# Kernel optimization log

Hardware: AMD Instinct MI355X
Metric: run time of the kernel (lower is better)

The kernel has to match this reference:

```python
import jax, jax.numpy as jnp
import numpy as np

ATTWSIZE = 64  # sliding window length (matches init_kwargs attwsize)


def setup_inputs() -> dict:
    key = jax.random.key(0)
    k1, k2, k3 = jax.random.split(key, 3)
    B, T, D, A = 32, 4096, 256, 128
    x = jax.random.normal(k1, (B, T, D), dtype=jnp.float32)
    Wp = jax.random.normal(k2, (A, D), dtype=jnp.float32) / np.sqrt(D).astype(np.float32)
    bp = jnp.zeros((A,), dtype=jnp.float32)
    Wg = jax.random.normal(k3, (1, A), dtype=jnp.float32) / np.sqrt(A).astype(np.float32)
    return {"x": x, "Wp": Wp, "bp": bp, "Wg": Wg}


def _windowed_sum(v, w):
    # causal sliding-window sum over axis=1: sum(v[:, max(t-w+1,0):t+1, :])
    # single-pass cumsum formulation: cs[t] - cs[t-w]
    cs = jnp.cumsum(v, axis=1)
    T = v.shape[1]
    shifted = jnp.pad(cs, ((0, 0), (w, 0), (0, 0)))[:, :T, :]
    return cs - shifted


def reference(x, Wp, bp, Wg):
    # proj = tanh(Linear(dimio->dimatt)(x))
    proj = jnp.tanh(jnp.einsum('btd,ad->bta', x, Wp) + bp)
    # gvec = sigmoid(Linear(dimatt->1, no bias)(proj))  -> [B, T, 1]
    g = jax.nn.sigmoid(jnp.einsum('bta,oa->bto', proj, Wg))
    wx = g * x  # gated input [B, T, D]
    num = _windowed_sum(wx, ATTWSIZE)         # [B, T, D]
    den = _windowed_sum(g, ATTWSIZE)          # [B, T, 1] broadcasts over D
    return num / den
```

## Files before the change

kernel.cpp:

```cpp
#include <hip/hip_runtime.h>

#define TT 4096
#define DD 256
#define AA 128
#define WIN 64

typedef short bf16x8 __attribute__((ext_vector_type(8)));
typedef float f32x4 __attribute__((ext_vector_type(4)));
typedef unsigned int u32x4 __attribute__((ext_vector_type(4)));

__device__ __forceinline__ unsigned short f2bf(float f) {
    unsigned int u = __builtin_bit_cast(unsigned int, f);
    u += 0x7FFFu + ((u >> 16) & 1u);
    return (unsigned short)(u >> 16);
}

__device__ __forceinline__ unsigned int cvt_pk_bf16(float lo, float hi) {
    unsigned int r;
    asm("v_cvt_pk_bf16_f32 %0, %1, %2" : "=v"(r) : "v"(lo), "v"(hi));
    return r;
}

__global__ __launch_bounds__(256) void prep_wp(const float* __restrict__ Wp,
                                               unsigned short* __restrict__ wpb) {
    int i = blockIdx.x * 256 + threadIdx.x;
    wpb[i] = f2bf(Wp[i]);
}

#define SROWS 32
#define TC    256
#define NU    ((TC + WIN) / SROWS)
#define NCHK  (TT / TC)

__global__ __launch_bounds__(256, 2) void fused_kernel(
        const float* __restrict__ x, const unsigned short* __restrict__ wpb,
        const float* __restrict__ bp, const float* __restrict__ Wg,
        float* __restrict__ out) {
    __shared__ __align__(16) float xs[2][SROWS * DD];
    __shared__ float gbuf[4][SROWS];
    __shared__ float psum[4][SROWS];
    const int tid  = threadIdx.x;
    const int lane = tid & 63;
    const int wave = tid >> 6;
    const int quad = lane >> 4;
    const int nrow = lane & 15;
    const int sw   = nrow & 7;
    const int b     = blockIdx.x >> 4;
    const int chunk = blockIdx.x & (NCHK - 1);
    const long t0   = (long)chunk * TC;
    const float* xb = x   + (size_t)b * TT * DD;
    float*       ob = out + (size_t)b * TT * DD;

    bf16x8 bfrag[2][8];
    float bpv[2], wgv[2];
#pragma unroll
    for (int nt = 0; nt < 2; ++nt) {
        int n = wave * 32 + nt * 16 + nrow;
        bpv[nt] = bp[n];
        wgv[nt] = Wg[n];
#pragma unroll
        for (int k0 = 0; k0 < 8; ++k0)
            bfrag[nt][k0] = *reinterpret_cast<const bf16x8*>(
                wpb + n * DD + k0 * 32 + quad * 8);
    }

    auto stage = [&](int su) {
        const int nb = su & 1;
        const long r0 = t0 - WIN + (long)su * SROWS;
#pragma unroll
        for (int j = 0; j < 8; ++j) {
            int r = wave * 8 + j;
            long row = r0 + r;
            row = row < 0 ? 0 : row;
            const float* gp = xb + row * DD + ((lane ^ (r & 7)) << 2);
            __builtin_amdgcn_global_load_lds(
                (const __attribute__((address_space(1))) void*)gp,
                (__attribute__((address_space(3))) void*)&xs[nb][r * DD],
                16, 0, 0);
        }
    };

    float S = 0.f, Sg = 0.f;

    stage(0);

    for (int u = 0; u <= NU; ++u) {
        if (u + 1 < NU) stage(u + 1);

        if (u + 1 < NU) asm volatile("s_waitcnt vmcnt(8) lgkmcnt(0)" ::: "memory");
        else            asm volatile("s_waitcnt vmcnt(0) lgkmcnt(0)" ::: "memory");
        __builtin_amdgcn_sched_barrier(0);
        __builtin_amdgcn_s_barrier();
        __builtin_amdgcn_sched_barrier(0);

        if (u < NU) {
            const float* buf = xs[u & 1];
            f32x4 acc[2][2];
#pragma unroll
            for (int mt = 0; mt < 2; ++mt)
#pragma unroll
                for (int nt = 0; nt < 2; ++nt)
                    acc[mt][nt] = (f32x4){0.f, 0.f, 0.f, 0.f};
#pragma unroll
            for (int k0 = 0; k0 < 8; ++k0) {
#pragma unroll
                for (int mt = 0; mt < 2; ++mt) {
                    const float* rowp = buf + (mt * 16 + nrow) * DD;
                    const int gidx = quad * 2 + k0 * 8;
                    float4 f0 = *reinterpret_cast<const float4*>(rowp + (((gidx)     ^ sw) << 2));
                    float4 f1 = *reinterpret_cast<const float4*>(rowp + (((gidx + 1) ^ sw) << 2));
                    u32x4 w;
                    w.x = cvt_pk_bf16(f0.x, f0.y);
                    w.y = cvt_pk_bf16(f0.z, f0.w);
                    w.z = cvt_pk_bf16(f1.x, f1.y);
                    w.w = cvt_pk_bf16(f1.z, f1.w);
                    bf16x8 af = __builtin_bit_cast(bf16x8, w);
                    acc[mt][0] = __builtin_amdgcn_mfma_f32_16x16x32_bf16(af, bfrag[0][k0], acc[mt][0], 0, 0, 0);
                    acc[mt][1] = __builtin_amdgcn_mfma_f32_16x16x32_bf16(af, bfrag[1][k0], acc[mt][1], 0, 0, 0);
                }
            }
            float p[2][4];
#pragma unroll
            for (int mt = 0; mt < 2; ++mt)
#pragma unroll
                for (int r = 0; r < 4; ++r) p[mt][r] = 0.f;
#pragma unroll
            for (int nt = 0; nt < 2; ++nt) {
#pragma unroll
                for (int mt = 0; mt < 2; ++mt) {
#pragma unroll
                    for (int r = 0; r < 4; ++r) {
                        float pre = acc[mt][nt][r] + bpv[nt];
                        float e  = __expf(2.0f * pre);
                        float th = 1.0f - 2.0f * __builtin_amdgcn_rcpf(e + 1.0f);
                        p[mt][r] += th * wgv[nt];
                    }
                }
            }
#pragma unroll
            for (int off = 1; off <= 8; off <<= 1)
#pragma unroll
                for (int mt = 0; mt < 2; ++mt)
#pragma unroll
                    for (int r = 0; r < 4; ++r)
                        p[mt][r] += __shfl_xor(p[mt][r], off, 64);
            if (nrow == 0) {
#pragma unroll
                for (int mt = 0; mt < 2; ++mt)
#pragma unroll
                    for (int r = 0; r < 4; ++r)
                        psum[wave][mt * 16 + quad * 4 + r] = p[mt][r];
            }
        }

        asm volatile("s_waitcnt lgkmcnt(0)" ::: "memory");
        __builtin_amdgcn_sched_barrier(0);
        __builtin_amdgcn_s_barrier();
        __builtin_amdgcn_sched_barrier(0);

        if (u < NU && tid < SROWS) {
            float ssum = psum[0][tid] + psum[1][tid] + psum[2][tid] + psum[3][tid];
            float gg = __builtin_amdgcn_rcpf(1.0f + __expf(-ssum));
            long row = t0 - WIN + (long)u * SROWS + tid;
            gbuf[u & 3][tid] = (row < 0) ? 0.f : gg;
        }

        if (u >= 1) {
            const int w = u - 1;
            const float* gn = gbuf[w & 3];
            const long rb = t0 - WIN + (long)w * SROWS;
            if (w >= 2) {
                const float* go = gbuf[(w + 2) & 3];
#pragma unroll 16
                for (int tt = 0; tt < SROWS; ++tt) {
                    long tn = rb + tt;
                    long to = tn - WIN;
                    to = to < 0 ? 0 : to;
                    float gnew = gn[tt];
                    float gold = go[tt];
                    float xn = xb[tn * DD + tid];
                    float xo = xb[to * DD + tid];
                    S  += gnew * xn - gold * xo;
                    Sg += gnew - gold;
                    ob[tn * DD + tid] = S * __builtin_amdgcn_rcpf(Sg);
                }
            } else {
#pragma unroll 16
                for (int tt = 0; tt < SROWS; ++tt) {
                    long rn = rb + tt;
                    rn = rn < 0 ? 0 : rn;
                    float gnew = gn[tt];
                    S  += gnew * xb[rn * DD + tid];
                    Sg += gnew;
                }
            }
        }
    }
}

extern "C" void kernel_launch(void* const* d_in, const int* in_sizes, int n_in,
                              void* d_out, int out_size, void* d_ws, size_t ws_size,
                              hipStream_t stream) {
    const float* x  = (const float*)d_in[0];
    const float* Wp = (const float*)d_in[1];
    const float* bp = (const float*)d_in[2];
    const float* Wg = (const float*)d_in[3];
    float* out = (float*)d_out;

    unsigned short* wpb = (unsigned short*)d_ws;

    prep_wp<<<AA * DD / 256, 256, 0, stream>>>(Wp, wpb);
    fused_kernel<<<32 * NCHK, 256, 0, stream>>>(x, wpb, bp, Wg, out);
}
```

Baseline: 270.7 us.

## Compute windowed sums from LDS tile with register cumsum history instead of global re-reads

The sliding-window stage now reads x from the LDS tile already staged for the GEMM rather than re-loading x rows (new and old) from global memory. It keeps a running cumulative sum with register-held history arrays (hA/hB, 32 floats each) so the window sum is cs minus the value from 64 rows earlier. The gate sigmoid is computed redundantly by every thread from a transposed psum layout, and the barrier/stage ordering is restructured. Outputs use nontemporal stores. The change removes the duplicate global traffic on x but adds 64 live registers per thread, which may pressure occupancy at 2 blocks per CU.

```diff
diff --git a/kernel.cpp b/kernel.cpp
--- a/kernel.cpp
+++ b/kernel.cpp
@@ -38,7 +38,7 @@
         float* __restrict__ out) {
     __shared__ __align__(16) float xs[2][SROWS * DD];
     __shared__ float gbuf[4][SROWS];
-    __shared__ float psum[4][SROWS];
+    __shared__ __align__(16) float psv[SROWS][4];
     const int tid  = threadIdx.x;
     const int lane = tid & 63;
     const int wave = tid >> 6;
@@ -80,77 +80,100 @@
         }
     };
 
-    float S = 0.f, Sg = 0.f;
+    float hA[SROWS], hB[SROWS];
+    float cs = 0.f, Sg = 0.f;
 
     stage(0);
 
-    for (int u = 0; u <= NU; ++u) {
+#define SBODY(H)                                                              \
+    _Pragma("unroll")                                                         \
+    for (int tt = 0; tt < SROWS; ++tt) {                                      \
+        long t = rbase + tt;                                                  \
+        f32x4 ps = *reinterpret_cast<const f32x4*>(&psv[tt][0]);              \
+        float ss = (ps[0] + ps[1]) + (ps[2] + ps[3]);                         \
+        float gnew = __builtin_amdgcn_rcpf(1.0f + __expf(-ss));               \
+        if (t < 0) gnew = 0.f;                                                \
+        if (tid == tt) gbuf[u & 3][tt] = gnew;                                \
+        int off = tt * DD + ((((tid >> 2) ^ (tt & 7)) << 2) | (tid & 3));     \
+        cs += gnew * xt[off];                                                 \
+        if (u >= 2) {                                                         \
+            float gold = gbuf[(u + 2) & 3][tt];                               \
+            Sg += gnew - gold;                                                \
+            float h = H[tt];                                                  \
+            H[tt] = cs;                                                       \
+            float o = (cs - h) * __builtin_amdgcn_rcpf(Sg);                   \
+            __builtin_nontemporal_store(o, &ob[t * DD + tid]);                \
+        } else {                                                              \
+            Sg += gnew;                                                       \
+            H[tt] = cs;                                                       \
+        }                                                                     \
+    }
+
+    for (int u = 0; u < NU; ++u) {
+        if (u >= 3) asm volatile("s_waitcnt vmcnt(32) lgkmcnt(0)" ::: "memory");
+        else        asm volatile("s_waitcnt vmcnt(0) lgkmcnt(0)"  ::: "memory");
+        __builtin_amdgcn_sched_barrier(0);
+        __builtin_amdgcn_s_barrier();
+        __builtin_amdgcn_sched_barrier(0);
+
         if (u + 1 < NU) stage(u + 1);
 
-        if (u + 1 < NU) asm volatile("s_waitcnt vmcnt(8) lgkmcnt(0)" ::: "memory");
-        else            asm volatile("s_waitcnt vmcnt(0) lgkmcnt(0)" ::: "memory");
-        __builtin_amdgcn_sched_barrier(0);
-        __builtin_amdgcn_s_barrier();
-        __builtin_amdgcn_sched_barrier(0);
-
-        if (u < NU) {
-            const float* buf = xs[u & 1];
-            f32x4 acc[2][2];
-#pragma unroll
-            for (int mt = 0; mt < 2; ++mt)
-#pragma unroll
-                for (int nt = 0; nt < 2; ++nt)
-                    acc[mt][nt] = (f32x4){0.f, 0.f, 0.f, 0.f};
-#pragma unroll
-            for (int k0 = 0; k0 < 8; ++k0) {
-#pragma unroll
-                for (int mt = 0; mt < 2; ++mt) {
-                    const float* rowp = buf + (mt * 16 + nrow) * DD;
-                    const int gidx = quad * 2 + k0 * 8;
-                    float4 f0 = *reinterpret_cast<const float4*>(rowp + (((gidx)     ^ sw) << 2));
-                    float4 f1 = *reinterpret_cast<const float4*>(rowp + (((gidx + 1) ^ sw) << 2));
-                    u32x4 w;
-                    w.x = cvt_pk_bf16(f0.x, f0.y);
-                    w.y = cvt_pk_bf16(f0.z, f0.w);
-                    w.z = cvt_pk_bf16(f1.x, f1.y);
-                    w.w = cvt_pk_bf16(f1.z, f1.w);
-                    bf16x8 af = __builtin_bit_cast(bf16x8, w);
-                    acc[mt][0] = __builtin_amdgcn_mfma_f32_16x16x32_bf16(af, bfrag[0][k0], acc[mt][0], 0, 0, 0);
-                    acc[mt][1] = __builtin_amdgcn_mfma_f32_16x16x32_bf16(af, bfrag[1][k0], acc[mt][1], 0, 0, 0);
+        const float* buf = xs[u & 1];
+        f32x4 acc[2][2];
+#pragma unroll
+        for (int mt = 0; mt < 2; ++mt)
+#pragma unroll
+            for (int nt = 0; nt < 2; ++nt)
+                acc[mt][nt] = (f32x4){0.f, 0.f, 0.f, 0.f};
+#pragma unroll
+        for (int k0 = 0; k0 < 8; ++k0) {
+#pragma unroll
+            for (int mt = 0; mt < 2; ++mt) {
+                const float* rowp = buf + (mt * 16 + nrow) * DD;
+                const int gidx = quad * 2 + k0 * 8;
+                float4 f0 = *reinterpret_cast<const float4*>(rowp + (((gidx)     ^ sw) << 2));
+                float4 f1 = *reinterpret_cast<const float4*>(rowp + (((gidx + 1) ^ sw) << 2));
+                u32x4 w;
+                w.x = cvt_pk_bf16(f0.x, f0.y);
+                w.y = cvt_pk_bf16(f0.z, f0.w);
+                w.z = cvt_pk_bf16(f1.x, f1.y);
+                w.w = cvt_pk_bf16(f1.z, f1.w);
+                bf16x8 af = __builtin_bit_cast(bf16x8, w);
+                acc[mt][0] = __builtin_amdgcn_mfma_f32_16x16x32_bf16(af, bfrag[0][k0], acc[mt][0], 0, 0, 0);
+                acc[mt][1] = __builtin_amdgcn_mfma_f32_16x16x32_bf16(af, bfrag[1][k0], acc[mt][1], 0, 0, 0);
+            }
+        }
+        float p[2][4];
+#pragma unroll
+        for (int mt = 0; mt < 2; ++mt)
+#pragma unroll
+            for (int r = 0; r < 4; ++r) p[mt][r] = 0.f;
+#pragma unroll
+        for (int nt = 0; nt < 2; ++nt) {
+#pragma unroll
+            for (int mt = 0; mt < 2; ++mt) {
+#pragma unroll
+                for (int r = 0; r < 4; ++r) {
+                    float pre = acc[mt][nt][r] + bpv[nt];
+                    float e  = __expf(2.0f * pre);
+                    float th = 1.0f - 2.0f * __builtin_amdgcn_rcpf(e + 1.0f);
+                    p[mt][r] += th * wgv[nt];
                 }
             }
-            float p[2][4];
+        }
+#pragma unroll
+        for (int off = 1; off <= 8; off <<= 1)
 #pragma unroll
             for (int mt = 0; mt < 2; ++mt)
 #pragma unroll
-                for (int r = 0; r < 4; ++r) p[mt][r] = 0.f;
-#pragma unroll
-            for (int nt = 0; nt < 2; ++nt) {
-#pragma unroll
-                for (int mt = 0; mt < 2; ++mt) {
-#pragma unroll
-                    for (int r = 0; r < 4; ++r) {
-                        float pre = acc[mt][nt][r] + bpv[nt];
-                        float e  = __expf(2.0f * pre);
-                        float th = 1.0f - 2.0f * __builtin_amdgcn_rcpf(e + 1.0f);
-                        p[mt][r] += th * wgv[nt];
-                    }
-                }
-            }
-#pragma unroll
-            for (int off = 1; off <= 8; off <<= 1)
-#pragma unroll
-                for (int mt = 0; mt < 2; ++mt)
-#pragma unroll
-                    for (int r = 0; r < 4; ++r)
-                        p[mt][r] += __shfl_xor(p[mt][r], off, 64);
-            if (nrow == 0) {
-#pragma unroll
-                for (int mt = 0; mt < 2; ++mt)
-#pragma unroll
-                    for (int r = 0; r < 4; ++r)
-                        psum[wave][mt * 16 + quad * 4 + r] = p[mt][r];
-            }
+                for (int r = 0; r < 4; ++r)
+                    p[mt][r] += __shfl_xor(p[mt][r], off, 64);
+        if (nrow == 0) {
+#pragma unroll
+            for (int mt = 0; mt < 2; ++mt)
+#pragma unroll
+                for (int r = 0; r < 4; ++r)
+                    psv[mt * 16 + quad * 4 + r][wave] = p[mt][r];
         }
 
         asm volatile("s_waitcnt lgkmcnt(0)" ::: "memory");
@@ -158,44 +181,13 @@
         __builtin_amdgcn_s_barrier();
         __builtin_amdgcn_sched_barrier(0);
 
-        if (u < NU && tid < SROWS) {
-            float ssum = psum[0][tid] + psum[1][tid] + psum[2][tid] + psum[3][tid];
-            float gg = __builtin_amdgcn_rcpf(1.0f + __expf(-ssum));
-            long row = t0 - WIN + (long)u * SROWS + tid;
-            gbuf[u & 3][tid] = (row < 0) ? 0.f : gg;
-        }
-
-        if (u >= 1) {
-            const int w = u - 1;
-            const float* gn = gbuf[w & 3];
-            const long rb = t0 - WIN + (long)w * SROWS;
-            if (w >= 2) {
-                const float* go = gbuf[(w + 2) & 3];
-#pragma unroll 16
-                for (int tt = 0; tt < SROWS; ++tt) {
-                    long tn = rb + tt;
-                    long to = tn - WIN;
-                    to = to < 0 ? 0 : to;
-                    float gnew = gn[tt];
-                    float gold = go[tt];
-                    float xn = xb[tn * DD + tid];
-                    float xo = xb[to * DD + tid];
-                    S  += gnew * xn - gold * xo;
-                    Sg += gnew - gold;
-                    ob[tn * DD + tid] = S * __builtin_amdgcn_rcpf(Sg);
-                }
-            } else {
-#pragma unroll 16
-                for (int tt = 0; tt < SROWS; ++tt) {
-                    long rn = rb + tt;
-                    rn = rn < 0 ? 0 : rn;
-                    float gnew = gn[tt];
-                    S  += gnew * xb[rn * DD + tid];
-                    Sg += gnew;
-                }
-            }
+        {
+            const long rbase = t0 - WIN + (long)u * SROWS;
+            const float* xt = xs[u & 1];
+            if (u & 1) { SBODY(hB) } else { SBODY(hA) }
         }
     }
+#undef SBODY
 }
 
 extern "C" void kernel_launch(void* const* d_in, const int* in_sizes, int n_in,
```

Result: slower. 311.3 us (+15.0%).
